# Kernel tuning notes

Hardware: AMD Instinct MI355X
Metric: run time of the kernel (lower is better)

## Reference

```python
import jax, jax.numpy as jnp
import numpy as np

FP8_MAX = 448.0  # float8_e4m3fn max


def _quant_fp8(x, scale):
    # static scaled fp8 quant: clamp to fp8 range, round via dtype cast
    q = jnp.clip(x / scale, -FP8_MAX, FP8_MAX).astype(jnp.float8_e4m3fn)
    return q.astype(jnp.float32)


def setup_inputs() -> dict:
    key = jax.random.key(0)
    ks = jax.random.split(key, 6)
    T, H = 8192, 4096
    I = 2 * H
    hidden_states = jax.random.normal(ks[0], (T, H), dtype=jnp.float32)
    residual = jax.random.normal(ks[1], (T, H), dtype=jnp.float32)
    norm_weight = jax.random.uniform(ks[2], (H,), dtype=jnp.float32)
    # fp8 weight: torch stores rand().to(fp8); emulate by rounding through fp8
    w_raw = jax.random.uniform(ks[3], (H, I), dtype=jnp.float32)  # already transposed [H, I]
    w = w_raw.astype(jnp.float8_e4m3fn).astype(jnp.float32)
    scale = jax.random.uniform(ks[4], (1,), dtype=jnp.float32) + 0.01
    wscale = jax.random.uniform(ks[5], (1,), dtype=jnp.float32) + 0.01
    return {"hidden_states": hidden_states, "residual": residual,
            "norm_weight": norm_weight, "w": w, "scale": scale, "wscale": wscale}


def reference(hidden_states, residual, norm_weight, w, scale, wscale):
    eps = 1e-6
    H = norm_weight.shape[0]
    x = hidden_states.reshape(-1, H)
    # tensor_model_parallel_all_reduce on a single device = identity
    all_reduce = x
    # fused add + RMSNorm (vllm RMSNorm with residual): residual_out = x + residual
    residual_out = all_reduce + residual
    var = jnp.mean(residual_out * residual_out, axis=-1, keepdims=True)
    norm_out = residual_out * jax.lax.rsqrt(var + eps) * norm_weight
    # static fp8 quant of activations, fp8 GEMM, dequant by scale*wscale
    q = _quant_fp8(norm_out, scale)  # [T, H]
    out = jnp.matmul(q, w) * (scale * wscale)  # [T, I]
    return (out, residual_out)
```

## Files before the change

### kernel.cpp

```cpp
#include <hip/hip_runtime.h>
#include <stdint.h>


typedef float float16v __attribute__((ext_vector_type(16)));
typedef int   int8v    __attribute__((ext_vector_type(8)));

#define GLOAD_LDS16(gp, lp)                                                    \
    __builtin_amdgcn_global_load_lds(                                          \
        (const __attribute__((address_space(1))) void*)(gp),                   \
        (__attribute__((address_space(3))) void*)(lp), 16, 0, 0)

#define MFMA_SCALE1(a, b, c)                                                   \
    __builtin_amdgcn_mfma_scale_f32_32x32x64_f8f6f4(                           \
        (a), (b), (c), 0, 0, 0, 0x7f7f7f7f, 0, 0x7f7f7f7f)

__global__ void __launch_bounds__(256) wconv_kernel(
    const float* __restrict__ w, uint8_t* __restrict__ wt, int K, int N) {
    __shared__ uint8_t tile[64 * 64];
    const int k0 = blockIdx.y * 64;
    const int n0 = blockIdx.x * 64;
    const int t = threadIdx.x;
    const int c4 = t & 15;
    const int r = t >> 4;

#pragma unroll
    for (int p = 0; p < 4; ++p) {
        const int k = r + p * 16;
        const float4 v = *(const float4*)(w + (size_t)(k0 + k) * N + n0 + c4 * 4);
        const int pk0 = __builtin_amdgcn_cvt_pk_fp8_f32(v.x, v.y, 0, false);
        const int pk1 = __builtin_amdgcn_cvt_pk_fp8_f32(v.z, v.w, 0, false);
        tile[(c4 * 4 + 0) * 64 + k] = (uint8_t)(pk0 & 0xff);
        tile[(c4 * 4 + 1) * 64 + k] = (uint8_t)((pk0 >> 8) & 0xff);
        tile[(c4 * 4 + 2) * 64 + k] = (uint8_t)(pk1 & 0xff);
        tile[(c4 * 4 + 3) * 64 + k] = (uint8_t)((pk1 >> 8) & 0xff);
    }
    __syncthreads();
    const int n_local = t >> 2;
    const int ch = t & 3;
    const uint4 val = *(const uint4*)(&tile[n_local * 64 + ch * 16]);
    const int n = n0 + n_local;
    const size_t tile_idx = (size_t)(n >> 7) * (K >> 6) + (k0 >> 6);
    const int c = ((n >> 5) & 3) * 4 + ch;
    *(uint4*)(wt + tile_idx * 8192 + c * 512 + (n & 31) * 16) = val;
}

__global__ void __launch_bounds__(256) norm_quant_kernel(
    const float* __restrict__ hs, const float* __restrict__ res,
    const float* __restrict__ nw, const float* __restrict__ scale,
    float* __restrict__ resid_out, uint8_t* __restrict__ q, int H) {
    __shared__ float sm[4096];
    __shared__ float wsum[4];
    __shared__ float s_inv;
    const int row = blockIdx.x;
    const int t = threadIdx.x;
    const float* hrow = hs + (size_t)row * H;
    const float* rrow = res + (size_t)row * H;
    float* orow = resid_out + (size_t)row * H;

    float acc = 0.f;
#pragma unroll
    for (int p = 0; p < 4; ++p) {
        const int c = p * 1024 + t * 4;
        const float4 h = *(const float4*)(hrow + c);
        const float4 r = *(const float4*)(rrow + c);
        float4 s;
        s.x = h.x + r.x; s.y = h.y + r.y; s.z = h.z + r.z; s.w = h.w + r.w;
        *(float4*)(orow + c) = s;
        *(float4*)(&sm[c]) = s;
        acc += s.x * s.x + s.y * s.y + s.z * s.z + s.w * s.w;
    }
#pragma unroll
    for (int off = 32; off; off >>= 1) acc += __shfl_down(acc, off);
    if ((t & 63) == 0) wsum[t >> 6] = acc;
    __syncthreads();
    if (t == 0) {
        const float tot = wsum[0] + wsum[1] + wsum[2] + wsum[3];
        s_inv = 1.0f / sqrtf(tot / (float)H + 1e-6f);
    }
    __syncthreads();
    const float inv = s_inv;
    const float sval = scale[0];

    const int k0 = t * 16;
    uint32_t words[4];
#pragma unroll
    for (int i = 0; i < 4; ++i) {
        const float4 s = *(const float4*)(&sm[k0 + i * 4]);
        const float4 wv = *(const float4*)(nw + k0 + i * 4);
        float q0 = (s.x * inv * wv.x) / sval;
        float q1 = (s.y * inv * wv.y) / sval;
        float q2 = (s.z * inv * wv.z) / sval;
        float q3 = (s.w * inv * wv.w) / sval;
        q0 = fminf(fmaxf(q0, -448.f), 448.f);
        q1 = fminf(fmaxf(q1, -448.f), 448.f);
        q2 = fminf(fmaxf(q2, -448.f), 448.f);
        q3 = fminf(fmaxf(q3, -448.f), 448.f);
        int pk = __builtin_amdgcn_cvt_pk_fp8_f32(q0, q1, 0, false);
        pk = __builtin_amdgcn_cvt_pk_fp8_f32(q2, q3, pk, true);
        words[i] = (uint32_t)pk;
    }
    const int kt = t >> 2;
    const int ch = t & 3;
    const size_t tile_idx = (size_t)(row >> 7) * (H >> 6) + kt;
    const int c = ((row >> 5) & 3) * 4 + ch;
    uint4 val;
    val.x = words[0]; val.y = words[1]; val.z = words[2]; val.w = words[3];
    *(uint4*)(q + tile_idx * 8192 + c * 512 + (row & 31) * 16) = val;
}

__global__ void __launch_bounds__(256) gemm_fp8_kernel(
    const uint8_t* __restrict__ A,
    const uint8_t* __restrict__ B,
    float* __restrict__ C,
    const float* __restrict__ scale, const float* __restrict__ wscale,
    int M, int N, int K) {
    __shared__ uint8_t lA[16384];
    __shared__ uint8_t lB[16384];

    const int t = threadIdx.x;
    const int wid = t >> 6;
    const int lane = t & 63;

    const int id = blockIdx.x;
    const int wg = (id & 7) * ((int)gridDim.x >> 3) + (id >> 3);
    const int nbn = N >> 7;
    const int bm = wg / nbn;
    const int bn = wg % nbn;

    const int wm = wid >> 1;
    const int wn = wid & 1;

    float16v acc[2][2] = {};

    const uint8_t* As = A + (size_t)bm * (K >> 6) * 8192;
    const uint8_t* Bs = B + (size_t)bn * (K >> 6) * 8192;

    const int lrow = (lane & 31) * 16;
    const int lgrp = (lane >> 5) * 1024;
    const int aoff0 = (wm * 2 + 0) * 2048 + lgrp + lrow;
    const int aoff1 = (wm * 2 + 1) * 2048 + lgrp + lrow;
    const int boff0 = (wn * 2 + 0) * 2048 + lgrp + lrow;
    const int boff1 = (wn * 2 + 1) * 2048 + lgrp + lrow;
    const int o16 = t * 16;

    const int nkt = K >> 7;
    for (int kt = 0; kt < nkt; ++kt) {
        GLOAD_LDS16(As + o16,         lA + o16);
        GLOAD_LDS16(As + 4096 + o16,  lA + 4096 + o16);
        GLOAD_LDS16(As + 8192 + o16,  lA + 8192 + o16);
        GLOAD_LDS16(As + 12288 + o16, lA + 12288 + o16);
        GLOAD_LDS16(Bs + o16,         lB + o16);
        GLOAD_LDS16(Bs + 4096 + o16,  lB + 4096 + o16);
        GLOAD_LDS16(Bs + 8192 + o16,  lB + 8192 + o16);
        GLOAD_LDS16(Bs + 12288 + o16, lB + 12288 + o16);
        As += 16384; Bs += 16384;
        __syncthreads();

#pragma unroll
        for (int half = 0; half < 2; ++half) {
            const int hb = half * 8192;
            const uint4 al0 = *(const uint4*)(lA + hb + aoff0);
            const uint4 ah0 = *(const uint4*)(lA + hb + aoff0 + 512);
            const uint4 al1 = *(const uint4*)(lA + hb + aoff1);
            const uint4 ah1 = *(const uint4*)(lA + hb + aoff1 + 512);
            const uint4 bl0 = *(const uint4*)(lB + hb + boff0);
            const uint4 bh0 = *(const uint4*)(lB + hb + boff0 + 512);
            const uint4 bl1 = *(const uint4*)(lB + hb + boff1);
            const uint4 bh1 = *(const uint4*)(lB + hb + boff1 + 512);
            const int8v a0 = {(int)al0.x, (int)al0.y, (int)al0.z, (int)al0.w,
                              (int)ah0.x, (int)ah0.y, (int)ah0.z, (int)ah0.w};
            const int8v a1 = {(int)al1.x, (int)al1.y, (int)al1.z, (int)al1.w,
                              (int)ah1.x, (int)ah1.y, (int)ah1.z, (int)ah1.w};
            const int8v b0 = {(int)bl0.x, (int)bl0.y, (int)bl0.z, (int)bl0.w,
                              (int)bh0.x, (int)bh0.y, (int)bh0.z, (int)bh0.w};
            const int8v b1 = {(int)bl1.x, (int)bl1.y, (int)bl1.z, (int)bl1.w,
                              (int)bh1.x, (int)bh1.y, (int)bh1.z, (int)bh1.w};
            acc[0][0] = MFMA_SCALE1(a0, b0, acc[0][0]);
            acc[0][1] = MFMA_SCALE1(a0, b1, acc[0][1]);
            acc[1][0] = MFMA_SCALE1(a1, b0, acc[1][0]);
            acc[1][1] = MFMA_SCALE1(a1, b1, acc[1][1]);
        }
        __syncthreads();
    }

    const float f = scale[0] * wscale[0];
    const int col = lane & 31;
    const int rbase = (lane >> 5) * 4;
#pragma unroll
    for (int i = 0; i < 2; ++i) {
#pragma unroll
        for (int j = 0; j < 2; ++j) {
#pragma unroll
            for (int reg = 0; reg < 16; ++reg) {
                const int r = (reg & 3) + 8 * (reg >> 2) + rbase;
                const size_t gr = (size_t)(bm * 128 + wm * 64 + i * 32 + r);
                const size_t gc = (size_t)(bn * 128 + wn * 64 + j * 32 + col);
                C[gr * N + gc] = acc[i][j][reg] * f;
            }
        }
    }
}

extern "C" void kernel_launch(void* const* d_in, const int* in_sizes, int n_in,
                              void* d_out, int out_size, void* d_ws, size_t ws_size,
                              hipStream_t stream) {
    const float* hs     = (const float*)d_in[0];
    const float* res    = (const float*)d_in[1];
    const float* nw     = (const float*)d_in[2];
    const float* w      = (const float*)d_in[3];
    const float* scale  = (const float*)d_in[4];
    const float* wscale = (const float*)d_in[5];

    const int H = in_sizes[2];
    const int T = in_sizes[0] / H;
    const int I = in_sizes[3] / H;

    float* out       = (float*)d_out;
    float* resid_out = out + (size_t)T * I;
    uint8_t* q  = (uint8_t*)d_ws;
    uint8_t* wt = q + (size_t)T * H;

    wconv_kernel<<<dim3(I / 64, H / 64), 256, 0, stream>>>(w, wt, H, I);
    norm_quant_kernel<<<T, 256, 0, stream>>>(hs, res, nw, scale, resid_out, q, H);
    gemm_fp8_kernel<<<(T / 128) * (I / 128), 256, 0, stream>>>(
        q, wt, out, scale, wscale, T, I, H);
}
```

Before: 469.6 us.

## Enlarge GEMM tile to 256x256 with triple-buffered async LDS prefetch

The fp8 GEMM moves from 128x128 tiles with 4 waves and synchronous load-then-compute to 256x256 tiles with 8 waves. It triple-buffers LDS so global-to-LDS loads for step k+2 run while step k computes, with one barrier per step. Loads are interleaved between MFMA groups, and s_setprio raises wave priority during the MFMAs. The aim is to hide global memory latency and raise data reuse per byte loaded, at the cost of 96KB of LDS per block, more accumulator registers, and fewer blocks in the grid.

```diff
diff --git a/kernel.cpp b/kernel.cpp
--- a/kernel.cpp
+++ b/kernel.cpp
@@ -108,94 +108,120 @@
     *(uint4*)(q + tile_idx * 8192 + c * 512 + (row & 31) * 16) = val;
 }
 
-__global__ void __launch_bounds__(256) gemm_fp8_kernel(
+static __device__ __forceinline__ int8v ldfrag(const uint8_t* p) {
+    const uint4 lo = *(const uint4*)p;
+    const uint4 hi = *(const uint4*)(p + 512);
+    int8v r = {(int)lo.x, (int)lo.y, (int)lo.z, (int)lo.w,
+               (int)hi.x, (int)hi.y, (int)hi.z, (int)hi.w};
+    return r;
+}
+
+__global__ void __launch_bounds__(512, 2) gemm_fp8_kernel(
     const uint8_t* __restrict__ A,
     const uint8_t* __restrict__ B,
     float* __restrict__ C,
     const float* __restrict__ scale, const float* __restrict__ wscale,
     int M, int N, int K) {
-    __shared__ uint8_t lA[16384];
-    __shared__ uint8_t lB[16384];
+    __shared__ uint8_t lds[3 * 32768];
 
     const int t = threadIdx.x;
     const int wid = t >> 6;
     const int lane = t & 63;
+    const int wr = wid >> 2;
+    const int wc = wid & 3;
 
     const int id = blockIdx.x;
     const int wg = (id & 7) * ((int)gridDim.x >> 3) + (id >> 3);
-    const int nbn = N >> 7;
+    const int nbn = N >> 8;
     const int bm = wg / nbn;
     const int bn = wg % nbn;
 
-    const int wm = wid >> 1;
-    const int wn = wid & 1;
-
-    float16v acc[2][2] = {};
-
-    const uint8_t* As = A + (size_t)bm * (K >> 6) * 8192;
-    const uint8_t* Bs = B + (size_t)bn * (K >> 6) * 8192;
-
+    const int nkt = K >> 6;
+    const uint8_t* a0s = A + (size_t)(2 * bm) * nkt * 8192;
+    const uint8_t* a1s = a0s + (size_t)nkt * 8192;
+    const uint8_t* b0s = B + (size_t)(2 * bn) * nkt * 8192;
+    const uint8_t* b1s = b0s + (size_t)nkt * 8192;
+    const int o16 = t * 16;
+
+#pragma unroll
+    for (int u = 0; u < 2; ++u) {
+        uint8_t* dst = lds + u * 32768;
+        const size_t ofs = (size_t)u * 8192 + o16;
+        GLOAD_LDS16(a0s + ofs, dst + o16);
+        GLOAD_LDS16(a1s + ofs, dst + 8192 + o16);
+        GLOAD_LDS16(b0s + ofs, dst + 16384 + o16);
+        GLOAD_LDS16(b1s + ofs, dst + 24576 + o16);
+    }
+
+    const int lgrp = (lane >> 5) * 1024;
     const int lrow = (lane & 31) * 16;
-    const int lgrp = (lane >> 5) * 1024;
-    const int aoff0 = (wm * 2 + 0) * 2048 + lgrp + lrow;
-    const int aoff1 = (wm * 2 + 1) * 2048 + lgrp + lrow;
-    const int boff0 = (wn * 2 + 0) * 2048 + lgrp + lrow;
-    const int boff1 = (wn * 2 + 1) * 2048 + lgrp + lrow;
-    const int o16 = t * 16;
-
-    const int nkt = K >> 7;
+    int aoff[4], boff[2];
+#pragma unroll
+    for (int mb = 0; mb < 4; ++mb) {
+        const int r32 = wr * 4 + mb;
+        aoff[mb] = (r32 >> 2) * 8192 + (r32 & 3) * 2048 + lgrp + lrow;
+    }
+#pragma unroll
+    for (int nb = 0; nb < 2; ++nb) {
+        const int c32 = wc * 2 + nb;
+        boff[nb] = 16384 + (c32 >> 2) * 8192 + (c32 & 3) * 2048 + lgrp + lrow;
+    }
+
+    float16v acc[4][2] = {};
+
+    int cur = 0, pfs = 2;
     for (int kt = 0; kt < nkt; ++kt) {
-        GLOAD_LDS16(As + o16,         lA + o16);
-        GLOAD_LDS16(As + 4096 + o16,  lA + 4096 + o16);
-        GLOAD_LDS16(As + 8192 + o16,  lA + 8192 + o16);
-        GLOAD_LDS16(As + 12288 + o16, lA + 12288 + o16);
-        GLOAD_LDS16(Bs + o16,         lB + o16);
-        GLOAD_LDS16(Bs + 4096 + o16,  lB + 4096 + o16);
-        GLOAD_LDS16(Bs + 8192 + o16,  lB + 8192 + o16);
-        GLOAD_LDS16(Bs + 12288 + o16, lB + 12288 + o16);
-        As += 16384; Bs += 16384;
-        __syncthreads();
-
-#pragma unroll
-        for (int half = 0; half < 2; ++half) {
-            const int hb = half * 8192;
-            const uint4 al0 = *(const uint4*)(lA + hb + aoff0);
-            const uint4 ah0 = *(const uint4*)(lA + hb + aoff0 + 512);
-            const uint4 al1 = *(const uint4*)(lA + hb + aoff1);
-            const uint4 ah1 = *(const uint4*)(lA + hb + aoff1 + 512);
-            const uint4 bl0 = *(const uint4*)(lB + hb + boff0);
-            const uint4 bh0 = *(const uint4*)(lB + hb + boff0 + 512);
-            const uint4 bl1 = *(const uint4*)(lB + hb + boff1);
-            const uint4 bh1 = *(const uint4*)(lB + hb + boff1 + 512);
-            const int8v a0 = {(int)al0.x, (int)al0.y, (int)al0.z, (int)al0.w,
-                              (int)ah0.x, (int)ah0.y, (int)ah0.z, (int)ah0.w};
-            const int8v a1 = {(int)al1.x, (int)al1.y, (int)al1.z, (int)al1.w,
-                              (int)ah1.x, (int)ah1.y, (int)ah1.z, (int)ah1.w};
-            const int8v b0 = {(int)bl0.x, (int)bl0.y, (int)bl0.z, (int)bl0.w,
-                              (int)bh0.x, (int)bh0.y, (int)bh0.z, (int)bh0.w};
-            const int8v b1 = {(int)bl1.x, (int)bl1.y, (int)bl1.z, (int)bl1.w,
-                              (int)bh1.x, (int)bh1.y, (int)bh1.z, (int)bh1.w};
-            acc[0][0] = MFMA_SCALE1(a0, b0, acc[0][0]);
-            acc[0][1] = MFMA_SCALE1(a0, b1, acc[0][1]);
-            acc[1][0] = MFMA_SCALE1(a1, b0, acc[1][0]);
-            acc[1][1] = MFMA_SCALE1(a1, b1, acc[1][1]);
-        }
-        __syncthreads();
+        asm volatile("s_waitcnt vmcnt(4)" ::: "memory");
+        __builtin_amdgcn_s_barrier();
+
+        const uint8_t* sl = lds + cur * 32768;
+        uint8_t* pdst = lds + pfs * 32768;
+        const int pf = (kt + 2 < nkt) ? (kt + 2) : (nkt - 1);
+        const size_t pofs = (size_t)pf * 8192 + o16;
+
+        const int8v b0 = ldfrag(sl + boff[0]);
+        const int8v b1 = ldfrag(sl + boff[1]);
+        const int8v a0 = ldfrag(sl + aoff[0]);
+        const int8v a1 = ldfrag(sl + aoff[1]);
+        GLOAD_LDS16(a0s + pofs, pdst + o16);
+        GLOAD_LDS16(a1s + pofs, pdst + 8192 + o16);
+        __builtin_amdgcn_sched_barrier(0);
+        __builtin_amdgcn_s_setprio(1);
+        acc[0][0] = MFMA_SCALE1(a0, b0, acc[0][0]);
+        acc[0][1] = MFMA_SCALE1(a0, b1, acc[0][1]);
+        acc[1][0] = MFMA_SCALE1(a1, b0, acc[1][0]);
+        acc[1][1] = MFMA_SCALE1(a1, b1, acc[1][1]);
+        __builtin_amdgcn_s_setprio(0);
+
+        const int8v a2 = ldfrag(sl + aoff[2]);
+        const int8v a3 = ldfrag(sl + aoff[3]);
+        GLOAD_LDS16(b0s + pofs, pdst + 16384 + o16);
+        GLOAD_LDS16(b1s + pofs, pdst + 24576 + o16);
+        __builtin_amdgcn_sched_barrier(0);
+        __builtin_amdgcn_s_setprio(1);
+        acc[2][0] = MFMA_SCALE1(a2, b0, acc[2][0]);
+        acc[2][1] = MFMA_SCALE1(a2, b1, acc[2][1]);
+        acc[3][0] = MFMA_SCALE1(a3, b0, acc[3][0]);
+        acc[3][1] = MFMA_SCALE1(a3, b1, acc[3][1]);
+        __builtin_amdgcn_s_setprio(0);
+
+        cur = (cur == 2) ? 0 : cur + 1;
+        pfs = (pfs == 2) ? 0 : pfs + 1;
     }
 
     const float f = scale[0] * wscale[0];
     const int col = lane & 31;
-    const int rbase = (lane >> 5) * 4;
-#pragma unroll
-    for (int i = 0; i < 2; ++i) {
-#pragma unroll
-        for (int j = 0; j < 2; ++j) {
+    const int rb4 = (lane >> 5) * 4;
+#pragma unroll
+    for (int mb = 0; mb < 4; ++mb) {
+#pragma unroll
+        for (int nb = 0; nb < 2; ++nb) {
 #pragma unroll
             for (int reg = 0; reg < 16; ++reg) {
-                const int r = (reg & 3) + 8 * (reg >> 2) + rbase;
-                const size_t gr = (size_t)(bm * 128 + wm * 64 + i * 32 + r);
-                const size_t gc = (size_t)(bn * 128 + wn * 64 + j * 32 + col);
-                C[gr * N + gc] = acc[i][j][reg] * f;
+                const int r = (reg & 3) + 8 * (reg >> 2) + rb4;
+                const size_t gr = (size_t)(bm * 256 + wr * 128 + mb * 32 + r);
+                const size_t gc = (size_t)(bn * 256 + wc * 64 + nb * 32 + col);
+                C[gr * N + gc] = acc[mb][nb][reg] * f;
             }
         }
     }
@@ -222,6 +248,6 @@
 
     wconv_kernel<<<dim3(I / 64, H / 64), 256, 0, stream>>>(w, wt, H, I);
     norm_quant_kernel<<<T, 256, 0, stream>>>(hs, res, nw, scale, resid_out, q, H);
-    gemm_fp8_kernel<<<(T / 128) * (I / 128), 256, 0, stream>>>(
+    gemm_fp8_kernel<<<(T / 256) * (I / 256), 512, 0, stream>>>(
         q, wt, out, scale, wscale, T, I, H);
 }
```

New measurement: 465.0 us. About the same (-1.0%).
